# Kernel optimization log

Measured on AMD Instinct MI355X. Metric: run time of the kernel, lower is better.

## Reference

```python
import jax, jax.numpy as jnp
import numpy as np

# ---- fixed problem dims (match init_kwargs) ----
B = 256            # graph pairs
NQ, NC = 96, 120   # nodes per query / corpus graph
EQ, EC = 192, 240  # edges per query / corpus graph
M = 256            # max_edge_set_size (pad target)
RAW = 32           # raw node/edge feature dim
H = 64             # node_state_dim
MSG = 128          # message_dim == encoded edge dim
SDIM = 64          # sinkhorn_feature_dim
PROP_STEPS = 3
TIME_STEPS = 2
SINK_ITERS = 10
TEMP = 0.1
N_NODES = B * (NQ + NC)
N_EDGES = B * (EQ + EC)


def _mlp2(x, W1, b1, W2, b2):
    return jax.nn.relu(x @ W1 + b1) @ W2 + b2


def _split_and_stack(ef):
    # edges laid out [q0, c0, q1, c1, ...]; pad each graph's edges to M
    D = ef.shape[-1]
    ef = ef.reshape(B, EQ + EC, D)
    q = jnp.pad(ef[:, :EQ], ((0, 0), (0, M - EQ), (0, 0)))
    c = jnp.pad(ef[:, EQ:], ((0, 0), (0, M - EC), (0, 0)))
    return q, c


def _sinkhorn(log_alpha):
    la = log_alpha / TEMP
    for _ in range(SINK_ITERS):
        la = la - jax.nn.logsumexp(la, axis=2, keepdims=True)
        la = la - jax.nn.logsumexp(la, axis=1, keepdims=True)
    return jnp.exp(la)


def setup_inputs() -> dict:
    key = jax.random.key(0)
    ks = jax.random.split(key, 16)
    rng = np.random.default_rng(0)
    nodes_per_graph = np.tile(np.array([NQ, NC]), B)            # [2B]
    node_offsets = np.concatenate([[0], np.cumsum(nodes_per_graph)[:-1]])
    edges_per_graph = np.tile(np.array([EQ, EC]), B)
    eg = np.repeat(np.arange(2 * B), edges_per_graph)           # graph id per edge
    from_idx = node_offsets[eg] + rng.integers(0, nodes_per_graph[eg])
    to_idx = node_offsets[eg] + rng.integers(0, nodes_per_graph[eg])

    def lin(k, i, o):
        return (jax.random.normal(k, (i, o), jnp.float32) / np.sqrt(i)).astype(jnp.float32)

    return {
        "node_features": jax.random.normal(ks[0], (N_NODES, RAW), jnp.float32),
        "edge_features": jax.random.normal(ks[1], (N_EDGES, RAW), jnp.float32),
        "from_idx": jnp.asarray(from_idx, jnp.int32),
        "to_idx": jnp.asarray(to_idx, jnp.int32),
        "enc_node_W": lin(ks[2], RAW, H), "enc_node_b": jnp.zeros((H,), jnp.float32),
        "enc_edge_W": lin(ks[3], RAW, MSG), "enc_edge_b": jnp.zeros((MSG,), jnp.float32),
        "msg_W1": lin(ks[4], 2 * H + MSG, 2 * MSG), "msg_b1": jnp.zeros((2 * MSG,), jnp.float32),
        "msg_W2": lin(ks[5], 2 * MSG, MSG), "msg_b2": jnp.zeros((MSG,), jnp.float32),
        "upd_W1": lin(ks[6], H + 2 * MSG, 2 * H), "upd_b1": jnp.zeros((2 * H,), jnp.float32),
        "upd_W2": lin(ks[7], 2 * H, H), "upd_b2": jnp.zeros((H,), jnp.float32),
        "int_W1": lin(ks[8], 2 * MSG, 2 * MSG), "int_b1": jnp.zeros((2 * MSG,), jnp.float32),
        "int_W2": lin(ks[9], 2 * MSG, MSG), "int_b2": jnp.zeros((MSG,), jnp.float32),
        "sink_W1": lin(ks[10], MSG, SDIM), "sink_b1": jnp.zeros((SDIM,), jnp.float32),
        "sink_W2": lin(ks[11], SDIM, SDIM), "sink_b2": jnp.zeros((SDIM,), jnp.float32),
    }


def _forward(node_features, edge_features,
             enc_node_W, enc_node_b, enc_edge_W, enc_edge_b,
             msg_W1, msg_b1, msg_W2, msg_b2,
             upd_W1, upd_b1, upd_W2, upd_b2,
             int_W1, int_b1, int_W2, int_b2,
             sink_W1, sink_b1, sink_W2, sink_b2,
             from_idx, to_idx):
    h0 = node_features @ enc_node_W + enc_node_b      # GraphEncoder (nodes)
    e0 = edge_features @ enc_edge_W + enc_edge_b      # GraphEncoder (edges) -> MSG dim
    mask_q = (jnp.arange(M) < EQ).astype(h0.dtype)[None, :, None]
    mask_c = (jnp.arange(M) < EC).astype(h0.dtype)[None, :, None]

    def edge_msgs(h, comb):
        hf, ht = h[from_idx], h[to_idx]
        mf = _mlp2(jnp.concatenate([hf, ht, comb], -1), msg_W1, msg_b1, msg_W2, msg_b2)
        mb = _mlp2(jnp.concatenate([ht, hf, comb], -1), msg_W1, msg_b1, msg_W2, msg_b2)
        return mf, mb

    plan = None
    q_store = c_store = None
    for _ in range(TIME_STEPS):
        h, e = h0, e0
        inter = jnp.zeros((N_EDGES, MSG), e0.dtype)
        for _ in range(PROP_STEPS):
            # interaction encoder on [edge_features_enc, interaction_features]
            comb = _mlp2(jnp.concatenate([e, inter], -1), int_W1, int_b1, int_W2, int_b2)
            # prop_layer: bidirectional messages + aggregation + node update
            mf, mb = edge_msgs(h, comb)
            agg_f = jax.ops.segment_sum(mf, to_idx, num_segments=N_NODES)
            agg_b = jax.ops.segment_sum(mb, from_idx, num_segments=N_NODES)
            h = _mlp2(jnp.concatenate([h, agg_f, agg_b], -1), upd_W1, upd_b1, upd_W2, upd_b2)
            # propagation_messages: per-edge messages from updated node states
            mf2, mb2 = edge_msgs(h, comb)
            e = mf2 + mb2
            # interaction features via transport-plan gather (zeros on first time step)
            if plan is None:
                inter = jnp.zeros((N_EDGES, MSG), e.dtype)
            else:
                qs, cs = _split_and_stack(e)
                q_int = jnp.einsum('bqc,bcd->bqd', plan, cs)[:, :EQ]
                c_int = jnp.einsum('bqc,bqd->bcd', plan, qs)[:, :EC]
                inter = jnp.concatenate([q_int, c_int], 1).reshape(N_EDGES, MSG)
        q_store, c_store = _split_and_stack(e)
        fq = _mlp2(q_store, sink_W1, sink_b1, sink_W2, sink_b2) * mask_q
        fc = _mlp2(c_store, sink_W1, sink_b1, sink_W2, sink_b2) * mask_c
        plan = _sinkhorn(jnp.einsum('bqd,bcd->bqc', fq, fc))
    # feature_alignment_score: -||Q - P C||_1 per pair
    return -jnp.abs(q_store - jnp.einsum('bqc,bcd->bqd', plan, c_store)).sum((1, 2))


def reference(node_features, edge_features, from_idx, to_idx,
              enc_node_W, enc_node_b, enc_edge_W, enc_edge_b,
              msg_W1, msg_b1, msg_W2, msg_b2,
              upd_W1, upd_b1, upd_W2, upd_b2,
              int_W1, int_b1, int_W2, int_b2,
              sink_W1, sink_b1, sink_W2, sink_b2):
    return _forward(node_features, edge_features,
                    enc_node_W, enc_node_b, enc_edge_W, enc_edge_b,
                    msg_W1, msg_b1, msg_W2, msg_b2,
                    upd_W1, upd_b1, upd_W2, upd_b2,
                    int_W1, int_b1, int_W2, int_b2,
                    sink_W1, sink_b1, sink_W2, sink_b2,
                    from_idx, to_idx)
```

## Files before the change

kernel.cpp:

```cpp
#include <hip/hip_runtime.h>
#include <math.h>

constexpr int BATCH = 256;
constexpr int EQ_   = 192;
constexpr int EC_   = 240;
constexpr int EPG   = 432;
constexpr int NPG   = 216;
constexpr int NN    = BATCH * NPG;
constexpr int NE    = BATCH * EPG;

typedef __attribute__((ext_vector_type(8))) short short8;
typedef __attribute__((ext_vector_type(4))) float floatx4;
typedef unsigned short u16;

__device__ __forceinline__ u16 f2bf(float x) {
  union { float f; unsigned u; } c; c.f = x;
  const unsigned r = (c.u + 0x7FFFu + ((c.u >> 16) & 1u)) >> 16;
  return (u16)r;
}
__device__ __forceinline__ float bf2f(u16 x) {
  union { unsigned u; float f; } c; c.u = ((unsigned)x) << 16;
  return c.f;
}
__device__ __forceinline__ unsigned pack2(float a, float b) {
  return (unsigned)f2bf(a) | ((unsigned)f2bf(b) << 16);
}
__device__ __forceinline__ short8 cvt8(const float* __restrict__ p) {
  const float4 a = *(const float4*)p;
  const float4 b = *(const float4*)(p + 4);
  short8 o;
  o[0]=(short)f2bf(a.x); o[1]=(short)f2bf(a.y); o[2]=(short)f2bf(a.z); o[3]=(short)f2bf(a.w);
  o[4]=(short)f2bf(b.x); o[5]=(short)f2bf(b.y); o[6]=(short)f2bf(b.z); o[7]=(short)f2bf(b.w);
  return o;
}

__device__ __forceinline__ void lse_online(float& m, float& s, float tt) {
  if (tt > m) { s = s * __expf(m - tt) + 1.f; m = tt; }
  else        { s += __expf(tt - m); }
}

__global__ __launch_bounds__(256)
void wconv(const float* __restrict__ W, u16* __restrict__ out, int K, int N)
{
  const int i = blockIdx.x * 256 + threadIdx.x;
  if (i < K * N) {
    const int n = i / K, k = i - n * K;
    out[i] = f2bf(W[(size_t)k * N + n]);
  }
}

template<int K1, int HID, int NOUT, int IN_MODE, int DUAL, int OUT_MODE, int WAVES>
__global__ __launch_bounds__(WAVES * 64, 4)
void mlp_mfma(const void* __restrict__ X, const void* __restrict__ P2,
              const void* __restrict__ P3, const u16* __restrict__ CB,
              const int* __restrict__ IA, const int* __restrict__ IB,
              const u16* __restrict__ W1t, const float* __restrict__ B1,
              const u16* __restrict__ W2t, const float* __restrict__ B2,
              float* __restrict__ Yf, u16* __restrict__ Yb0, u16* __restrict__ Yb1)
{
  constexpr int RT  = 32;
  constexpr int THREADS = WAVES * 64;
  constexpr int KCH = K1 / 8;
  constexpr int NT1 = HID / (WAVES * 16);
  constexpr int NT2 = (NOUT / (WAVES * 16) > 0) ? NOUT / (WAVES * 16) : 1;
  constexpr int SAB = RT * K1 * 2;
  constexpr int SHB = RT * (HID + 8) * 2;
  __shared__ __align__(16) char smem[(SAB > SHB ? SAB : SHB)];
  u16* sA = (u16*)smem;
  u16* sH = (u16*)smem;

  const int tid = threadIdx.x;
  const int rowBase = blockIdx.x * RT;

  for (int ch = tid; ch < RT * KCH; ch += THREADS) {
    const int r = ch / KCH, kc = ch - r * KCH;
    const int gr = rowBase + r, k0 = kc * 8;
    short8 pk;
    if constexpr (IN_MODE == 4) {
      const float* Xf  = (const float*)X;
      const float* P2f = (const float*)P2;
      if (k0 < 128)      pk = cvt8(&Xf[(size_t)gr * 128 + k0]);
      else if (P2f)      pk = cvt8(&P2f[(size_t)gr * 128 + (k0 - 128)]);
      else { pk = short8{0,0,0,0,0,0,0,0}; }
    } else if constexpr (IN_MODE == 1) {
      const u16* Hb = (const u16*)X;
      if (k0 < 64)       pk = *(const short8*)&Hb[(size_t)IA[gr] * 64 + k0];
      else if (k0 < 128) pk = *(const short8*)&Hb[(size_t)IB[gr] * 64 + (k0 - 64)];
      else               pk = *(const short8*)&CB[(size_t)gr * 128 + (k0 - 128)];
    } else {
      const u16* Hb = (const u16*)X;
      const u16* A0 = (const u16*)P2;
      const u16* A1 = (const u16*)P3;
      if (k0 < 64)       pk = *(const short8*)&Hb[(size_t)gr * 64 + k0];
      else if (k0 < 192) pk = *(const short8*)&A0[(size_t)gr * 128 + (k0 - 64)];
      else               pk = *(const short8*)&A1[(size_t)gr * 128 + (k0 - 192)];
    }
    const int byte = ((r * K1 + k0) * 2) ^ ((r & 7) << 4);
    *(short8*)((char*)sA + byte) = pk;
  }
  __syncthreads();

  const int wid = tid >> 6, lane = tid & 63;
  const int l15 = lane & 15, lg = lane >> 4;

  floatx4 acc1[1 + DUAL][2][NT1];
  #pragma unroll
  for (int d = 0; d <= DUAL; ++d)
    #pragma unroll
    for (int m = 0; m < 2; ++m)
      #pragma unroll
      for (int n = 0; n < NT1; ++n) acc1[d][m][n] = floatx4{0.f,0.f,0.f,0.f};

  #pragma unroll 2
  for (int kk = 0; kk < K1 / 32; ++kk) {
    short8 bw[NT1];
    #pragma unroll
    for (int n = 0; n < NT1; ++n) {
      const int col = wid * (HID / WAVES) + n * 16 + l15;
      bw[n] = *(const short8*)&W1t[(size_t)col * K1 + kk * 32 + lg * 8];
    }
    #pragma unroll
    for (int d = 0; d <= DUAL; ++d) {
      int k0 = kk * 32 + lg * 8;
      if (DUAL && d && k0 < 128) k0 ^= 64;
      #pragma unroll
      for (int m = 0; m < 2; ++m) {
        const int r = m * 16 + l15;
        const int byte = ((r * K1 + k0) * 2) ^ ((r & 7) << 4);
        const short8 af = *(const short8*)((char*)sA + byte);
        #pragma unroll
        for (int n = 0; n < NT1; ++n)
          acc1[d][m][n] = __builtin_amdgcn_mfma_f32_16x16x32_bf16(af, bw[n], acc1[d][m][n], 0, 0, 0);
      }
    }
  }
  __syncthreads();

  floatx4 accO[2][NT2];
  #pragma unroll
  for (int m = 0; m < 2; ++m)
    #pragma unroll
    for (int n = 0; n < NT2; ++n) accO[m][n] = floatx4{0.f,0.f,0.f,0.f};

  #pragma unroll
  for (int d = 0; d <= DUAL; ++d) {
    #pragma unroll
    for (int n = 0; n < NT1; ++n) {
      const int col = wid * (HID / WAVES) + n * 16 + l15;
      const float b1 = B1[col];
      #pragma unroll
      for (int m = 0; m < 2; ++m)
        #pragma unroll
        for (int r = 0; r < 4; ++r) {
          const int row = m * 16 + lg * 4 + r;
          const float y = acc1[d][m][n][r] + b1;
          sH[row * (HID + 8) + col] = f2bf(y > 0.f ? y : 0.f);
        }
    }
    __syncthreads();
    if (OUT_MODE == 2 && d == 1) {
      #pragma unroll
      for (int m = 0; m < 2; ++m)
        #pragma unroll
        for (int n = 0; n < NT2; ++n) accO[m][n] = floatx4{0.f,0.f,0.f,0.f};
    }
    #pragma unroll 2
    for (int kk = 0; kk < HID / 32; ++kk) {
      short8 bw2[NT2];
      #pragma unroll
      for (int n = 0; n < NT2; ++n) {
        const int col = wid * (NOUT / WAVES) + n * 16 + l15;
        bw2[n] = *(const short8*)&W2t[(size_t)col * HID + kk * 32 + lg * 8];
      }
      #pragma unroll
      for (int m = 0; m < 2; ++m) {
        const short8 af = *(const short8*)&sH[(m * 16 + l15) * (HID + 8) + kk * 32 + lg * 8];
        #pragma unroll
        for (int n = 0; n < NT2; ++n)
          accO[m][n] = __builtin_amdgcn_mfma_f32_16x16x32_bf16(af, bw2[n], accO[m][n], 0, 0, 0);
      }
    }
    if constexpr (OUT_MODE == 2) {
      u16* Y = d ? Yb1 : Yb0;
      #pragma unroll
      for (int n = 0; n < NT2; ++n) {
        const int col = wid * (NOUT / WAVES) + n * 16 + l15;
        const float b2 = B2[col];
        #pragma unroll
        for (int m = 0; m < 2; ++m)
          #pragma unroll
          for (int r = 0; r < 4; ++r) {
            const int gr = rowBase + m * 16 + lg * 4 + r;
            Y[(size_t)gr * NOUT + col] = f2bf(accO[m][n][r] + b2);
          }
      }
    }
    if (DUAL && d == 0) __syncthreads();
  }

  if constexpr (OUT_MODE != 2) {
    #pragma unroll
    for (int n = 0; n < NT2; ++n) {
      const int col = wid * (NOUT / WAVES) + n * 16 + l15;
      const float b2 = B2[col] * (float)(1 + DUAL);
      #pragma unroll
      for (int m = 0; m < 2; ++m)
        #pragma unroll
        for (int r = 0; r < 4; ++r) {
          const int gr = rowBase + m * 16 + lg * 4 + r;
          const float y = accO[m][n][r] + b2;
          if constexpr (OUT_MODE == 1) {
            Yb0[(size_t)gr * NOUT + col] = f2bf(y);
          } else {
            Yf[(size_t)gr * NOUT + col] = y;
            if constexpr (OUT_MODE == 3)
              Yb0[(size_t)gr * NOUT + col] = f2bf(y);
          }
        }
    }
  }
}

template<int EBF16>
__global__ __launch_bounds__(512, 4)
void comb_msg_fused(const void* __restrict__ E, const u16* __restrict__ INTER,
                    const u16* __restrict__ Hb,
                    const int* __restrict__ IA, const int* __restrict__ IB,
                    const u16* __restrict__ Wi1, const float* __restrict__ Bi1,
                    const u16* __restrict__ Wi2, const float* __restrict__ Bi2,
                    const u16* __restrict__ Wm1, const float* __restrict__ Bm1,
                    const u16* __restrict__ Wm2, const float* __restrict__ Bm2,
                    u16* __restrict__ COMB, u16* __restrict__ MI)
{
  constexpr int RT = 32;
  __shared__ __align__(16) char smem[RT * (256 + 8) * 2];
  u16* sA = (u16*)smem;
  u16* sH = (u16*)smem;

  const int tid = threadIdx.x;
  const int rowBase = blockIdx.x * RT;
  const int wid = tid >> 6, lane = tid & 63;
  const int l15 = lane & 15, lg = lane >> 4;

  for (int ch = tid; ch < RT * 32; ch += 512) {
    const int r = ch >> 5, kc = ch & 31;
    const int gr = rowBase + r, k0 = kc * 8;
    short8 pk;
    if (k0 < 128) {
      if constexpr (EBF16) pk = *(const short8*)&((const u16*)E)[(size_t)gr * 128 + k0];
      else                 pk = cvt8(&((const float*)E)[(size_t)gr * 128 + k0]);
    }
    else if (INTER) pk = *(const short8*)&INTER[(size_t)gr * 128 + (k0 - 128)];
    else            pk = short8{0,0,0,0,0,0,0,0};
    const int byte = ((r * 256 + k0) * 2) ^ ((r & 7) << 4);
    *(short8*)((char*)sA + byte) = pk;
  }
  __syncthreads();

  floatx4 c1[2][2];
  #pragma unroll
  for (int m = 0; m < 2; ++m) { c1[m][0] = floatx4{0,0,0,0}; c1[m][1] = floatx4{0,0,0,0}; }
  #pragma unroll 2
  for (int kk = 0; kk < 8; ++kk) {
    short8 bw[2];
    #pragma unroll
    for (int n = 0; n < 2; ++n) {
      const int col = wid * 32 + n * 16 + l15;
      bw[n] = *(const short8*)&Wi1[(size_t)col * 256 + kk * 32 + lg * 8];
    }
    #pragma unroll
    for (int m = 0; m < 2; ++m) {
      const int r = m * 16 + l15;
      const int byte = ((r * 256 + kk * 32 + lg * 8) * 2) ^ ((r & 7) << 4);
      const short8 af = *(const short8*)((char*)sA + byte);
      c1[m][0] = __builtin_amdgcn_mfma_f32_16x16x32_bf16(af, bw[0], c1[m][0], 0, 0, 0);
      c1[m][1] = __builtin_amdgcn_mfma_f32_16x16x32_bf16(af, bw[1], c1[m][1], 0, 0, 0);
    }
  }
  __syncthreads();
  #pragma unroll
  for (int n = 0; n < 2; ++n) {
    const int col = wid * 32 + n * 16 + l15;
    const float b1 = Bi1[col];
    #pragma unroll
    for (int m = 0; m < 2; ++m)
      #pragma unroll
      for (int r = 0; r < 4; ++r) {
        const int row = m * 16 + lg * 4 + r;
        const float y = c1[m][n][r] + b1;
        sH[row * 264 + col] = f2bf(y > 0.f ? y : 0.f);
      }
  }
  __syncthreads();
  floatx4 cO[2];
  cO[0] = floatx4{0,0,0,0}; cO[1] = floatx4{0,0,0,0};
  #pragma unroll 2
  for (int kk = 0; kk < 8; ++kk) {
    const int col = wid * 16 + l15;
    const short8 bw2 = *(const short8*)&Wi2[(size_t)col * 256 + kk * 32 + lg * 8];
    #pragma unroll
    for (int m = 0; m < 2; ++m) {
      const short8 af = *(const short8*)&sH[(m * 16 + l15) * 264 + kk * 32 + lg * 8];
      cO[m] = __builtin_amdgcn_mfma_f32_16x16x32_bf16(af, bw2, cO[m], 0, 0, 0);
    }
  }
  __syncthreads();

  {
    const int col = wid * 16 + l15;
    const float b2 = Bi2[col];
    #pragma unroll
    for (int m = 0; m < 2; ++m)
      #pragma unroll
      for (int r = 0; r < 4; ++r) {
        const int row = m * 16 + lg * 4 + r;
        const int gr = rowBase + row;
        const u16 v = f2bf(cO[m][r] + b2);
        COMB[(size_t)gr * 128 + col] = v;
        const int k0 = 128 + col;
        const int byte = ((row * 256 + k0) * 2) ^ ((row & 7) << 4);
        *(u16*)((char*)sA + byte) = v;
      }
  }
  for (int ch = tid; ch < RT * 16; ch += 512) {
    const int r = ch >> 4, kc = ch & 15;
    const int gr = rowBase + r, k0 = kc * 8;
    short8 pk;
    if (k0 < 64) pk = *(const short8*)&Hb[(size_t)IA[gr] * 64 + k0];
    else         pk = *(const short8*)&Hb[(size_t)IB[gr] * 64 + (k0 - 64)];
    const int byte = ((r * 256 + k0) * 2) ^ ((r & 7) << 4);
    *(short8*)((char*)sA + byte) = pk;
  }
  __syncthreads();

  floatx4 m1[2][2][2];
  #pragma unroll
  for (int d = 0; d < 2; ++d)
    #pragma unroll
    for (int m = 0; m < 2; ++m) { m1[d][m][0] = floatx4{0,0,0,0}; m1[d][m][1] = floatx4{0,0,0,0}; }
  #pragma unroll 2
  for (int kk = 0; kk < 8; ++kk) {
    short8 bw[2];
    #pragma unroll
    for (int n = 0; n < 2; ++n) {
      const int col = wid * 32 + n * 16 + l15;
      bw[n] = *(const short8*)&Wm1[(size_t)col * 256 + kk * 32 + lg * 8];
    }
    #pragma unroll
    for (int d = 0; d < 2; ++d) {
      int k0 = kk * 32 + lg * 8;
      if (d && k0 < 128) k0 ^= 64;
      #pragma unroll
      for (int m = 0; m < 2; ++m) {
        const int r = m * 16 + l15;
        const int byte = ((r * 256 + k0) * 2) ^ ((r & 7) << 4);
        const short8 af = *(const short8*)((char*)sA + byte);
        m1[d][m][0] = __builtin_amdgcn_mfma_f32_16x16x32_bf16(af, bw[0], m1[d][m][0], 0, 0, 0);
        m1[d][m][1] = __builtin_amdgcn_mfma_f32_16x16x32_bf16(af, bw[1], m1[d][m][1], 0, 0, 0);
      }
    }
  }
  __syncthreads();

  floatx4 mO[2];
  #pragma unroll
  for (int d = 0; d < 2; ++d) {
    #pragma unroll
    for (int n = 0; n < 2; ++n) {
      const int col = wid * 32 + n * 16 + l15;
      const float b1 = Bm1[col];
      #pragma unroll
      for (int m = 0; m < 2; ++m)
        #pragma unroll
        for (int r = 0; r < 4; ++r) {
          const int row = m * 16 + lg * 4 + r;
          const float y = m1[d][m][n][r] + b1;
          sH[row * 264 + col] = f2bf(y > 0.f ? y : 0.f);
        }
    }
    __syncthreads();
    mO[0] = floatx4{0,0,0,0}; mO[1] = floatx4{0,0,0,0};
    #pragma unroll 2
    for (int kk = 0; kk < 8; ++kk) {
      const int col = wid * 16 + l15;
      const short8 bw2 = *(const short8*)&Wm2[(size_t)col * 256 + kk * 32 + lg * 8];
      #pragma unroll
      for (int m = 0; m < 2; ++m) {
        const short8 af = *(const short8*)&sH[(m * 16 + l15) * 264 + kk * 32 + lg * 8];
        mO[m] = __builtin_amdgcn_mfma_f32_16x16x32_bf16(af, bw2, mO[m], 0, 0, 0);
      }
    }
    {
      const int col = wid * 16 + l15;
      const float b2 = Bm2[col];
      #pragma unroll
      for (int m = 0; m < 2; ++m)
        #pragma unroll
        for (int r = 0; r < 4; ++r) {
          const int gr = rowBase + m * 16 + lg * 4 + r;
          MI[(size_t)gr * 256 + d * 128 + col] = f2bf(mO[m][r] + b2);
        }
    }
    if (d == 0) __syncthreads();
  }
}

__global__ __launch_bounds__(512)
void scatter_agg(const u16* __restrict__ MI,
                 const int* __restrict__ FI, const int* __restrict__ TI,
                 u16* __restrict__ AggF, u16* __restrict__ AggB)
{
  const int pair = blockIdx.x >> 1, dir = blockIdx.x & 1;
  const int* SI = dir ? FI : TI;
  u16* Agg      = dir ? AggB : AggF;
  const int tid = threadIdx.x;
  __shared__ float sAgg[NPG * 128];

  for (int i = tid; i < NPG * 128; i += 512) sAgg[i] = 0.f;
  __syncthreads();

  for (int i = tid; i < EPG * 32; i += 512) {
    const int edge = i >> 5, cb = i & 31;
    const int er = pair * EPG + edge;
    const int node = SI[er] - pair * NPG;
    const size_t base = (size_t)er * 256 + dir * 128 + cb;
    #pragma unroll
    for (int k = 0; k < 4; ++k)
      atomicAdd(&sAgg[node * 128 + cb + 32 * k], bf2f(MI[base + 32 * k]));
  }
  __syncthreads();
  unsigned* dst = (unsigned*)(Agg + (size_t)pair * NPG * 128);
  for (int i = tid; i < NPG * 64; i += 512)
    dst[i] = pack2(sAgg[2 * i], sAgg[2 * i + 1]);
}

template<int K1, int HID, int NOUT, int IN_MODE, int SINGLE, int OUTBF>
__global__ __launch_bounds__(256)
void fused_mlp(const float* __restrict__ X, const float* __restrict__ P1,
               const float* __restrict__ W1, const float* __restrict__ B1,
               const float* __restrict__ W2, const float* __restrict__ B2,
               float* __restrict__ Y, u16* __restrict__ Yb, int maskLen)
{
  constexpr int RT = 32, BK = 32;
  constexpr int J1 = HID / 32;
  constexpr int J2 = NOUT / 32;
  constexpr int BMAX = (HID > NOUT ? HID : NOUT);
  __shared__ float sA[RT * 33];
  __shared__ float sB[BK * BMAX];
  __shared__ float sH[SINGLE ? 1 : RT * (HID + 1)];

  const int t  = threadIdx.x;
  const int tx = t & 31, ty = t >> 5;
  const int rowBase = blockIdx.x * RT;

  float acc[4][J1];
  #pragma unroll
  for (int i = 0; i < 4; ++i)
    #pragma unroll
    for (int j = 0; j < J1; ++j) acc[i][j] = 0.f;

  for (int kb = 0; kb < K1; kb += BK) {
    for (int l = t; l < RT * BK; l += 256) {
      const int r = l >> 5, k = l & 31;
      const int gr = rowBase + r, gk = kb + k;
      float v;
      if constexpr (IN_MODE == 0) {
        v = X[(size_t)gr * K1 + gk];
      } else {
        const int bb = gr >> 8, m = gr & 255;
        constexpr int off = (IN_MODE == 5) ? 0 : EQ_;
        constexpr int len = (IN_MODE == 5) ? EQ_ : EC_;
        v = (m < len) ? P1[((size_t)bb * EPG + off + m) * 128 + gk] : 0.f;
      }
      sA[r * 33 + k] = v;
    }
    for (int l = t * 4; l < BK * HID; l += 1024) {
      *(float4*)&sB[l] = *(const float4*)&W1[(size_t)(kb + l / HID) * HID + (l % HID)];
    }
    __syncthreads();
    #pragma unroll
    for (int k = 0; k < BK; ++k) {
      const float a0 = sA[(ty*4+0)*33+k], a1 = sA[(ty*4+1)*33+k],
                  a2 = sA[(ty*4+2)*33+k], a3 = sA[(ty*4+3)*33+k];
      #pragma unroll
      for (int j = 0; j < J1; ++j) {
        const float bb = sB[k * HID + tx + 32*j];
        acc[0][j] += a0 * bb; acc[1][j] += a1 * bb;
        acc[2][j] += a2 * bb; acc[3][j] += a3 * bb;
      }
    }
    __syncthreads();
  }

  if constexpr (SINGLE) {
    #pragma unroll
    for (int j = 0; j < J1; ++j) {
      const int col = tx + 32*j;
      const float bias = B1[col];
      #pragma unroll
      for (int i = 0; i < 4; ++i) {
        const int gr = rowBase + ty*4 + i;
        if constexpr (OUTBF) Yb[(size_t)gr * HID + col] = f2bf(acc[i][j] + bias);
        else                 Y[(size_t)gr * HID + col] = acc[i][j] + bias;
      }
    }
  } else {
    #pragma unroll
    for (int j = 0; j < J1; ++j) {
      const int col = tx + 32*j;
      const float bias = B1[col];
      #pragma unroll
      for (int i = 0; i < 4; ++i) {
        float y = acc[i][j] + bias;
        sH[(ty*4+i) * (HID+1) + col] = y > 0.f ? y : 0.f;
      }
    }
    __syncthreads();

    float acc2[4][J2];
    #pragma unroll
    for (int i = 0; i < 4; ++i)
      #pragma unroll
      for (int j = 0; j < J2; ++j) acc2[i][j] = 0.f;

    for (int kb = 0; kb < HID; kb += BK) {
      for (int l = t * 4; l < BK * NOUT; l += 1024) {
        *(float4*)&sB[l] = *(const float4*)&W2[(size_t)(kb + l / NOUT) * NOUT + (l % NOUT)];
      }
      __syncthreads();
      #pragma unroll
      for (int k = 0; k < BK; ++k) {
        const float a0 = sH[(ty*4+0)*(HID+1) + kb + k],
                    a1 = sH[(ty*4+1)*(HID+1) + kb + k],
                    a2 = sH[(ty*4+2)*(HID+1) + kb + k],
                    a3 = sH[(ty*4+3)*(HID+1) + kb + k];
        #pragma unroll
        for (int j = 0; j < J2; ++j) {
          const float bb = sB[k * NOUT + tx + 32*j];
          acc2[0][j] += a0 * bb; acc2[1][j] += a1 * bb;
          acc2[2][j] += a2 * bb; acc2[3][j] += a3 * bb;
        }
      }
      __syncthreads();
    }
    #pragma unroll
    for (int j = 0; j < J2; ++j) {
      const int col = tx + 32*j;
      const float bias = B2[col];
      #pragma unroll
      for (int i = 0; i < 4; ++i) {
        const int gr = rowBase + ty*4 + i;
        float y = acc2[i][j] + bias;
        if (maskLen >= 0 && (gr & 255) >= maskLen) y = 0.f;
        Y[(size_t)gr * NOUT + col] = y;
      }
    }
  }
}

__global__ __launch_bounds__(256)
void gemm_nt_scale(const float* __restrict__ A, const float* __restrict__ Bm,
                   float* __restrict__ C, float scale)
{
  const int b = blockIdx.z, qt = blockIdx.x, ct = blockIdx.y;
  __shared__ float sA[64 * 68];
  __shared__ float sB[64 * 68];
  const int t = threadIdx.x;
  const int tx = t & 15, ty = t >> 4;
  const float* Ab = A  + (size_t)b * 16384 + (size_t)qt * 4096;
  const float* Bb = Bm + (size_t)b * 16384 + (size_t)ct * 4096;
  for (int l = t * 4; l < 64 * 64; l += 1024) {
    const int r = l >> 6, d = l & 63;
    *(float4*)&sA[r*68 + d] = *(const float4*)&Ab[r*64 + d];
    *(float4*)&sB[r*68 + d] = *(const float4*)&Bb[r*64 + d];
  }
  __syncthreads();
  float acc[4][4] = {};
  #pragma unroll
  for (int d = 0; d < 64; ++d) {
    float a[4], bb[4];
    #pragma unroll
    for (int i = 0; i < 4; ++i) a[i]  = sA[(ty*4+i)*68 + d];
    #pragma unroll
    for (int j = 0; j < 4; ++j) bb[j] = sB[(tx+16*j)*68 + d];
    #pragma unroll
    for (int i = 0; i < 4; ++i)
      #pragma unroll
      for (int j = 0; j < 4; ++j) acc[i][j] += a[i] * bb[j];
  }
  float* Cb = C + (size_t)b * 65536 + (size_t)(qt*64) * 256 + ct*64;
  #pragma unroll
  for (int i = 0; i < 4; ++i)
    #pragma unroll
    for (int j = 0; j < 4; ++j)
      Cb[(ty*4+i)*256 + tx + 16*j] = acc[i][j] * scale;
}

template<int TRANSA, int EBF16, int OUTBF>
__global__ __launch_bounds__(256)
void gemm_plan_mfma(const float* __restrict__ P, const void* __restrict__ E,
                    void* __restrict__ Y, int RPB, int YOFF, int VOFF,
                    int VLEN, int maskRows)
{
  __shared__ u16 sP[64 * 40];
  __shared__ u16 sVT[128 * 40];
  const int b = blockIdx.y, rt = blockIdx.x;
  const int t = threadIdx.x;
  const int wid = t >> 6, lane = t & 63;
  const int l15 = lane & 15, lg = lane >> 4;
  const float* Pb = P + (size_t)b * 65536;

  floatx4 acc[8];
  #pragma unroll
  for (int n = 0; n < 8; ++n) acc[n] = floatx4{0.f,0.f,0.f,0.f};

  for (int kb = 0; kb < 256; kb += 32) {
    if constexpr (TRANSA == 0) {
      for (int l = t; l < 64 * 32; l += 256) {
        const int r = l >> 5, k = l & 31;
        sP[r * 40 + k] = f2bf(Pb[(size_t)(rt * 64 + r) * 256 + kb + k]);
      }
    } else {
      for (int l = t; l < 64 * 32; l += 256) {
        const int q = l >> 6, c = l & 63;
        sP[c * 40 + q] = f2bf(Pb[(size_t)(kb + q) * 256 + rt * 64 + c]);
      }
    }
    for (int l = t; l < 32 * 128; l += 256) {
      const int k = l >> 7, d = l & 127;
      const int vr = kb + k;
      u16 v = 0;
      if (vr < VLEN) {
        if constexpr (EBF16) v = ((const u16*)E)[((size_t)b * EPG + VOFF + vr) * 128 + d];
        else                 v = f2bf(((const float*)E)[((size_t)b * EPG + VOFF + vr) * 128 + d]);
      }
      sVT[d * 40 + k] = v;
    }
    __syncthreads();
    const short8 af = *(const short8*)&sP[(wid * 16 + l15) * 40 + lg * 8];
    #pragma unroll
    for (int n = 0; n < 8; ++n) {
      const short8 bw = *(const short8*)&sVT[(n * 16 + l15) * 40 + lg * 8];
      acc[n] = __builtin_amdgcn_mfma_f32_16x16x32_bf16(af, bw, acc[n], 0, 0, 0);
    }
    __syncthreads();
  }
  #pragma unroll
  for (int n = 0; n < 8; ++n) {
    const int col = n * 16 + l15;
    #pragma unroll
    for (int r = 0; r < 4; ++r) {
      const int row = rt * 64 + wid * 16 + lg * 4 + r;
      if (row < maskRows) {
        const size_t idx = ((size_t)b * RPB + YOFF + row) * 128 + col;
        if constexpr (OUTBF) ((u16*)Y)[idx] = f2bf(acc[n][r]);
        else                 ((float*)Y)[idx] = acc[n][r];
      }
    }
  }
}

__global__ __launch_bounds__(1024)
void sinkhorn_fused(float* __restrict__ S)
{
  const int b = blockIdx.x, t = threadIdx.x;
  float* Sb = S + (size_t)b * 65536;
  const int w = t >> 6, lane = t & 63;
  const int cbase = lane * 4;
  __shared__ float pm[16 * 256], ps[16 * 256];
  __shared__ float su[256], sv[256];
  if (t < 256) sv[t] = 0.f;
  __syncthreads();

  for (int it = 0; it < 10; ++it) {
    const float4 v4 = *(const float4*)&sv[cbase];
    float4 cm = {-1e30f, -1e30f, -1e30f, -1e30f};
    float4 cs = {0.f, 0.f, 0.f, 0.f};
    #pragma unroll 2
    for (int i = 0; i < 16; ++i) {
      const int r = w * 16 + i;
      const float4 s4 = *(const float4*)&Sb[(size_t)r * 256 + cbase];
      const float ax = s4.x + v4.x, ay = s4.y + v4.y;
      const float az = s4.z + v4.z, aw = s4.w + v4.w;
      float m = fmaxf(fmaxf(ax, ay), fmaxf(az, aw));
      #pragma unroll
      for (int off = 32; off; off >>= 1) m = fmaxf(m, __shfl_xor(m, off));
      float s = __expf(ax - m) + __expf(ay - m) + __expf(az - m) + __expf(aw - m);
      #pragma unroll
      for (int off = 32; off; off >>= 1) s += __shfl_xor(s, off);
      const float u = -(m + __logf(s));
      if (lane == 0) su[r] = u;
      lse_online(cm.x, cs.x, s4.x + u);
      lse_online(cm.y, cs.y, s4.y + u);
      lse_online(cm.z, cs.z, s4.z + u);
      lse_online(cm.w, cs.w, s4.w + u);
    }
    *(float4*)&pm[w * 256 + cbase] = cm;
    *(float4*)&ps[w * 256 + cbase] = cs;
    __syncthreads();
    if (t < 256) {
      float m = pm[t];
      #pragma unroll
      for (int k = 1; k < 16; ++k) m = fmaxf(m, pm[k * 256 + t]);
      float s = 0.f;
      #pragma unroll
      for (int k = 0; k < 16; ++k) s += ps[k * 256 + t] * __expf(pm[k * 256 + t] - m);
      sv[t] = -(m + __logf(s));
    }
    __syncthreads();
  }
  for (int i = t; i < 16384; i += 1024) {
    const int row = i >> 6, c4 = (i & 63) * 4;
    float4 s4 = *(float4*)&Sb[(size_t)row * 256 + c4];
    const float uu = su[row];
    const float4 v4 = *(const float4*)&sv[c4];
    s4.x = __expf(s4.x + uu + v4.x);
    s4.y = __expf(s4.y + uu + v4.y);
    s4.z = __expf(s4.z + uu + v4.z);
    s4.w = __expf(s4.w + uu + v4.w);
    *(float4*)&Sb[(size_t)row * 256 + c4] = s4;
  }
}

__global__ __launch_bounds__(256)
void escore_kernel(const float* __restrict__ e, const float* __restrict__ pc,
                   float* __restrict__ out)
{
  const int b = blockIdx.x, t = threadIdx.x;
  float acc = 0.f;
  for (int i4 = t; i4 < 8192; i4 += 256) {
    const int flat = i4 * 4;
    const int m = flat >> 7, d = flat & 127;
    float4 p = *(const float4*)&pc[((size_t)b * 256 + m) * 128 + d];
    float4 q = {0.f, 0.f, 0.f, 0.f};
    if (m < EQ_) q = *(const float4*)&e[((size_t)b * EPG + m) * 128 + d];
    acc += fabsf(q.x - p.x) + fabsf(q.y - p.y) + fabsf(q.z - p.z) + fabsf(q.w - p.w);
  }
  __shared__ float red[256];
  red[t] = acc; __syncthreads();
  for (int s2 = 128; s2 > 0; s2 >>= 1) { if (t < s2) red[t] += red[t + s2]; __syncthreads(); }
  if (t == 0) out[b] = -red[0];
}

extern "C" void kernel_launch(void* const* d_in, const int* in_sizes, int n_in,
                              void* d_out, int out_size, void* d_ws, size_t ws_size,
                              hipStream_t stream)
{
  const float* node_features = (const float*)d_in[0];
  const float* edge_features = (const float*)d_in[1];
  const int*   from_idx      = (const int*)d_in[2];
  const int*   to_idx        = (const int*)d_in[3];
  const float* enc_node_W = (const float*)d_in[4];
  const float* enc_node_b = (const float*)d_in[5];
  const float* enc_edge_W = (const float*)d_in[6];
  const float* enc_edge_b = (const float*)d_in[7];
  const float* msg_W1 = (const float*)d_in[8];
  const float* msg_b1 = (const float*)d_in[9];
  const float* msg_W2 = (const float*)d_in[10];
  const float* msg_b2 = (const float*)d_in[11];
  const float* upd_W1 = (const float*)d_in[12];
  const float* upd_b1 = (const float*)d_in[13];
  const float* upd_W2 = (const float*)d_in[14];
  const float* upd_b2 = (const float*)d_in[15];
  const float* int_W1 = (const float*)d_in[16];
  const float* int_b1 = (const float*)d_in[17];
  const float* int_W2 = (const float*)d_in[18];
  const float* int_b2 = (const float*)d_in[19];
  const float* sink_W1 = (const float*)d_in[20];
  const float* sink_b1 = (const float*)d_in[21];
  const float* sink_W2 = (const float*)d_in[22];
  const float* sink_b2 = (const float*)d_in[23];
  float* out = (float*)d_out;

  u16* wsu = (u16*)d_ws;
  u16*   hb  = wsu;
  float* e   = (float*)(wsu + (size_t)NN * 64);
  float* shr = e + (size_t)NE * 128;
  float* S   = shr + (size_t)BATCH * 32768;
  u16* comb  = (u16*)(S + (size_t)BATCH * 65536);
  u16* e1b   = comb + (size_t)NE * 128;
  u16* h1b   = e1b + (size_t)NE * 128;
  u16* wi1 = h1b + (size_t)NN * 64;
  u16* wi2 = wi1 + 65536;
  u16* wm1 = wi2 + 32768;
  u16* wm2 = wm1 + 65536;
  u16* wu1 = wm2 + 32768;
  u16* wu2 = wu1 + 40960;

  u16* mI = (u16*)e;
  u16* interb = (u16*)shr;
  u16* aggFb  = (u16*)shr;
  u16* aggBb  = aggFb + (size_t)NN * 128;
  float* fq   = shr;
  float* fc   = shr + (size_t)BATCH * 16384;
  float* pc   = shr;

  wconv<<<256, 256, 0, stream>>>(int_W1, wi1, 256, 256);
  wconv<<<128, 256, 0, stream>>>(int_W2, wi2, 256, 128);
  wconv<<<256, 256, 0, stream>>>(msg_W1, wm1, 256, 256);
  wconv<<<128, 256, 0, stream>>>(msg_W2, wm2, 256, 128);
  wconv<<<160, 256, 0, stream>>>(upd_W1, wu1, 320, 128);
  wconv<<< 32, 256, 0, stream>>>(upd_W2, wu2, 128, 64);

  fused_mlp<32,64,64,0,1,1><<<NN/32, 256, 0, stream>>>(
      node_features, nullptr, enc_node_W, enc_node_b, nullptr, nullptr,
      nullptr, hb, -1);
  fused_mlp<32,128,128,0,1,0><<<NE/32, 256, 0, stream>>>(
      edge_features, nullptr, enc_edge_W, enc_edge_b, nullptr, nullptr,
      e, nullptr, -1);

  for (int p = 0; p < 3; ++p) {
    comb_msg_fused<0><<<NE/32, 512, 0, stream>>>(
        e, nullptr, hb, from_idx, to_idx,
        wi1, int_b1, wi2, int_b2, wm1, msg_b1, wm2, msg_b2, comb, mI);
    scatter_agg<<<BATCH*2, 512, 0, stream>>>(mI, from_idx, to_idx, aggFb, aggBb);
    mlp_mfma<320,128,64,3,0,1,4><<<NN/32, 256, 0, stream>>>(
        hb, aggFb, aggBb, nullptr, nullptr, nullptr,
        wu1, upd_b1, wu2, upd_b2, nullptr, hb, nullptr);
    if (p == 0) {
      hipMemcpyAsync(h1b, hb, (size_t)NN * 64 * 2, hipMemcpyDeviceToDevice, stream);
      mlp_mfma<256,256,128,1,1,3,8><<<NE/32, 512, 0, stream>>>(
          hb, nullptr, nullptr, comb, from_idx, to_idx,
          wm1, msg_b1, wm2, msg_b2, e, e1b, nullptr);
    } else {
      mlp_mfma<256,256,128,1,1,0,8><<<NE/32, 512, 0, stream>>>(
          hb, nullptr, nullptr, comb, from_idx, to_idx,
          wm1, msg_b1, wm2, msg_b2, e, nullptr, nullptr);
    }
  }
  fused_mlp<128,64,64,5,0,0><<<BATCH*8, 256, 0, stream>>>(
      nullptr, e, sink_W1, sink_b1, sink_W2, sink_b2, fq, nullptr, EQ_);
  fused_mlp<128,64,64,6,0,0><<<BATCH*8, 256, 0, stream>>>(
      nullptr, e, sink_W1, sink_b1, sink_W2, sink_b2, fc, nullptr, EC_);
  gemm_nt_scale<<<dim3(4,4,BATCH), 256, 0, stream>>>(fq, fc, S, 10.0f);
  sinkhorn_fused<<<BATCH, 1024, 0, stream>>>(S);

  hipMemcpyAsync(hb, h1b, (size_t)NN * 64 * 2, hipMemcpyDeviceToDevice, stream);
  gemm_plan_mfma<0,1,1><<<dim3(4, BATCH), 256, 0, stream>>>(
      S, e1b, interb, EPG, 0,   EQ_, EC_, EQ_);
  gemm_plan_mfma<1,1,1><<<dim3(4, BATCH), 256, 0, stream>>>(
      S, e1b, interb, EPG, EQ_, 0,   EQ_, EC_);

  comb_msg_fused<1><<<NE/32, 512, 0, stream>>>(
      e1b, interb, hb, from_idx, to_idx,
      wi1, int_b1, wi2, int_b2, wm1, msg_b1, wm2, msg_b2, comb, mI);
  scatter_agg<<<BATCH*2, 512, 0, stream>>>(mI, from_idx, to_idx, aggFb, aggBb);
  mlp_mfma<320,128,64,3,0,1,4><<<NN/32, 256, 0, stream>>>(
      hb, aggFb, aggBb, nullptr, nullptr, nullptr,
      wu1, upd_b1, wu2, upd_b2, nullptr, hb, nullptr);
  mlp_mfma<256,256,128,1,1,0,8><<<NE/32, 512, 0, stream>>>(
      hb, nullptr, nullptr, comb, from_idx, to_idx,
      wm1, msg_b1, wm2, msg_b2, e, nullptr, nullptr);
  gemm_plan_mfma<0,0,1><<<dim3(4, BATCH), 256, 0, stream>>>(
      S, e, interb, EPG, 0,   EQ_, EC_, EQ_);
  gemm_plan_mfma<1,0,1><<<dim3(4, BATCH), 256, 0, stream>>>(
      S, e, interb, EPG, EQ_, 0,   EQ_, EC_);

  comb_msg_fused<0><<<NE/32, 512, 0, stream>>>(
      e, interb, hb, from_idx, to_idx,
      wi1, int_b1, wi2, int_b2, wm1, msg_b1, wm2, msg_b2, comb, mI);
  scatter_agg<<<BATCH*2, 512, 0, stream>>>(mI, from_idx, to_idx, aggFb, aggBb);
  mlp_mfma<320,128,64,3,0,1,4><<<NN/32, 256, 0, stream>>>(
      hb, aggFb, aggBb, nullptr, nullptr, nullptr,
      wu1, upd_b1, wu2, upd_b2, nullptr, hb, nullptr);
  mlp_mfma<256,256,128,1,1,0,8><<<NE/32, 512, 0, stream>>>(
      hb, nullptr, nullptr, comb, from_idx, to_idx,
      wm1, msg_b1, wm2, msg_b2, e, nullptr, nullptr);

  fused_mlp<128,64,64,5,0,0><<<BATCH*8, 256, 0, stream>>>(
      nullptr, e, sink_W1, sink_b1, sink_W2, sink_b2, fq, nullptr, EQ_);
  fused_mlp<128,64,64,6,0,0><<<BATCH*8, 256, 0, stream>>>(
      nullptr, e, sink_W1, sink_b1, sink_W2, sink_b2, fc, nullptr, EC_);
  gemm_nt_scale<<<dim3(4,4,BATCH), 256, 0, stream>>>(fq, fc, S, 10.0f);
  sinkhorn_fused<<<BATCH, 1024, 0, stream>>>(S);

  gemm_plan_mfma<0,0,0><<<dim3(4, BATCH), 256, 0, stream>>>(
      S, e, pc, 256, 0, EQ_, EC_, 256);
  escore_kernel<<<BATCH, 256, 0, stream>>>(e, pc, out);
}
```

Baseline: 3.492 ms.

## Run Sinkhorn feature MLP on MFMA with split-bf16 and simplify column LSE

Replaces the fp32 SIMT two-layer Sinkhorn feature MLP with an MFMA kernel. It splits both activations and weights into bf16 hi/lo parts and uses three MFMAs per tile to approximate fp32 accuracy. It also drops the online max tracking in the Sinkhorn column logsumexp and sums exp(s+u) directly. This relies on values being bounded after row normalization, which removes per-element branching and max reductions. The risks are a small loss of precision in the MLP and possible underflow or overflow in the column sums.

Measured after the change: 3.271 ms. 6.3% less time.

```diff
diff --git a/kernel.cpp b/kernel.cpp
--- a/kernel.cpp
+++ b/kernel.cpp
@@ -46,6 +46,20 @@
   if (i < K * N) {
     const int n = i / K, k = i - n * K;
     out[i] = f2bf(W[(size_t)k * N + n]);
+  }
+}
+
+__global__ __launch_bounds__(256)
+void wconv_split(const float* __restrict__ W, u16* __restrict__ hi,
+                 u16* __restrict__ lo, int K, int N)
+{
+  const int i = blockIdx.x * 256 + threadIdx.x;
+  if (i < K * N) {
+    const int n = i / K, k = i - n * K;
+    const float w = W[(size_t)k * N + n];
+    const u16 h = f2bf(w);
+    hi[i] = h;
+    lo[i] = f2bf(w - bf2f(h));
   }
 }
 
@@ -504,57 +518,108 @@
         else                 Y[(size_t)gr * HID + col] = acc[i][j] + bias;
       }
     }
-  } else {
-    #pragma unroll
-    for (int j = 0; j < J1; ++j) {
-      const int col = tx + 32*j;
-      const float bias = B1[col];
-      #pragma unroll
-      for (int i = 0; i < 4; ++i) {
-        float y = acc[i][j] + bias;
-        sH[(ty*4+i) * (HID+1) + col] = y > 0.f ? y : 0.f;
-      }
-    }
-    __syncthreads();
-
-    float acc2[4][J2];
-    #pragma unroll
-    for (int i = 0; i < 4; ++i)
-      #pragma unroll
-      for (int j = 0; j < J2; ++j) acc2[i][j] = 0.f;
-
-    for (int kb = 0; kb < HID; kb += BK) {
-      for (int l = t * 4; l < BK * NOUT; l += 1024) {
-        *(float4*)&sB[l] = *(const float4*)&W2[(size_t)(kb + l / NOUT) * NOUT + (l % NOUT)];
-      }
-      __syncthreads();
-      #pragma unroll
-      for (int k = 0; k < BK; ++k) {
-        const float a0 = sH[(ty*4+0)*(HID+1) + kb + k],
-                    a1 = sH[(ty*4+1)*(HID+1) + kb + k],
-                    a2 = sH[(ty*4+2)*(HID+1) + kb + k],
-                    a3 = sH[(ty*4+3)*(HID+1) + kb + k];
-        #pragma unroll
-        for (int j = 0; j < J2; ++j) {
-          const float bb = sB[k * NOUT + tx + 32*j];
-          acc2[0][j] += a0 * bb; acc2[1][j] += a1 * bb;
-          acc2[2][j] += a2 * bb; acc2[3][j] += a3 * bb;
-        }
-      }
-      __syncthreads();
-    }
-    #pragma unroll
-    for (int j = 0; j < J2; ++j) {
-      const int col = tx + 32*j;
-      const float bias = B2[col];
-      #pragma unroll
-      for (int i = 0; i < 4; ++i) {
-        const int gr = rowBase + ty*4 + i;
-        float y = acc2[i][j] + bias;
-        if (maskLen >= 0 && (gr & 255) >= maskLen) y = 0.f;
-        Y[(size_t)gr * NOUT + col] = y;
-      }
-    }
+  }
+}
+
+template<int OFFSET, int LEN>
+__global__ __launch_bounds__(256)
+void sink_mlp_split(const float* __restrict__ E,
+                    const u16* __restrict__ W1hi, const u16* __restrict__ W1lo,
+                    const float* __restrict__ B1,
+                    const u16* __restrict__ W2hi, const u16* __restrict__ W2lo,
+                    const float* __restrict__ B2,
+                    float* __restrict__ Y)
+{
+  __shared__ u16 sAhi[32 * 136], sAlo[32 * 136];
+  __shared__ u16 sHhi[32 * 72],  sHlo[32 * 72];
+  const int tid = threadIdx.x;
+  const int rowBase = blockIdx.x * 32;
+
+  for (int ch = tid; ch < 32 * 16; ch += 256) {
+    const int r = ch >> 4, kc = ch & 15;
+    const int gr = rowBase + r, k0 = kc * 8;
+    const int b = gr >> 8, m = gr & 255;
+    short8 hi, lo;
+    if (m < LEN) {
+      const float* src = &E[((size_t)b * EPG + OFFSET + m) * 128 + k0];
+      #pragma unroll
+      for (int j = 0; j < 8; ++j) {
+        const float v = src[j];
+        const u16 h = f2bf(v);
+        hi[j] = (short)h;
+        lo[j] = (short)f2bf(v - bf2f(h));
+      }
+    } else {
+      hi = short8{0,0,0,0,0,0,0,0};
+      lo = short8{0,0,0,0,0,0,0,0};
+    }
+    *(short8*)&sAhi[r * 136 + k0] = hi;
+    *(short8*)&sAlo[r * 136 + k0] = lo;
+  }
+  __syncthreads();
+
+  const int wid = tid >> 6, lane = tid & 63;
+  const int l15 = lane & 15, lg = lane >> 4;
+  const int col = wid * 16 + l15;
+
+  floatx4 acc[2];
+  acc[0] = floatx4{0,0,0,0}; acc[1] = floatx4{0,0,0,0};
+  #pragma unroll
+  for (int kk = 0; kk < 4; ++kk) {
+    const short8 bh = *(const short8*)&W1hi[(size_t)col * 128 + kk * 32 + lg * 8];
+    const short8 bl = *(const short8*)&W1lo[(size_t)col * 128 + kk * 32 + lg * 8];
+    #pragma unroll
+    for (int m = 0; m < 2; ++m) {
+      const int r = m * 16 + l15;
+      const short8 ahi = *(const short8*)&sAhi[r * 136 + kk * 32 + lg * 8];
+      const short8 alo = *(const short8*)&sAlo[r * 136 + kk * 32 + lg * 8];
+      acc[m] = __builtin_amdgcn_mfma_f32_16x16x32_bf16(ahi, bh, acc[m], 0, 0, 0);
+      acc[m] = __builtin_amdgcn_mfma_f32_16x16x32_bf16(ahi, bl, acc[m], 0, 0, 0);
+      acc[m] = __builtin_amdgcn_mfma_f32_16x16x32_bf16(alo, bh, acc[m], 0, 0, 0);
+    }
+  }
+  {
+    const float b1 = B1[col];
+    #pragma unroll
+    for (int m = 0; m < 2; ++m)
+      #pragma unroll
+      for (int r4 = 0; r4 < 4; ++r4) {
+        const int row = m * 16 + lg * 4 + r4;
+        float y = acc[m][r4] + b1;
+        y = y > 0.f ? y : 0.f;
+        const u16 h = f2bf(y);
+        sHhi[row * 72 + col] = h;
+        sHlo[row * 72 + col] = f2bf(y - bf2f(h));
+      }
+  }
+  __syncthreads();
+  floatx4 acc2[2];
+  acc2[0] = floatx4{0,0,0,0}; acc2[1] = floatx4{0,0,0,0};
+  #pragma unroll
+  for (int kk = 0; kk < 2; ++kk) {
+    const short8 bh = *(const short8*)&W2hi[(size_t)col * 64 + kk * 32 + lg * 8];
+    const short8 bl = *(const short8*)&W2lo[(size_t)col * 64 + kk * 32 + lg * 8];
+    #pragma unroll
+    for (int m = 0; m < 2; ++m) {
+      const int r = m * 16 + l15;
+      const short8 ahi = *(const short8*)&sHhi[r * 72 + kk * 32 + lg * 8];
+      const short8 alo = *(const short8*)&sHlo[r * 72 + kk * 32 + lg * 8];
+      acc2[m] = __builtin_amdgcn_mfma_f32_16x16x32_bf16(ahi, bh, acc2[m], 0, 0, 0);
+      acc2[m] = __builtin_amdgcn_mfma_f32_16x16x32_bf16(ahi, bl, acc2[m], 0, 0, 0);
+      acc2[m] = __builtin_amdgcn_mfma_f32_16x16x32_bf16(alo, bh, acc2[m], 0, 0, 0);
+    }
+  }
+  {
+    const float b2 = B2[col];
+    #pragma unroll
+    for (int m = 0; m < 2; ++m)
+      #pragma unroll
+      for (int r4 = 0; r4 < 4; ++r4) {
+        const int gr = rowBase + m * 16 + lg * 4 + r4;
+        float y = acc2[m][r4] + b2;
+        if ((gr & 255) >= LEN) y = 0.f;
+        Y[(size_t)gr * 64 + col] = y;
+      }
   }
 }
 
@@ -667,14 +732,13 @@
   float* Sb = S + (size_t)b * 65536;
   const int w = t >> 6, lane = t & 63;
   const int cbase = lane * 4;
-  __shared__ float pm[16 * 256], ps[16 * 256];
+  __shared__ float ps[16 * 256];
   __shared__ float su[256], sv[256];
   if (t < 256) sv[t] = 0.f;
   __syncthreads();
 
   for (int it = 0; it < 10; ++it) {
     const float4 v4 = *(const float4*)&sv[cbase];
-    float4 cm = {-1e30f, -1e30f, -1e30f, -1e30f};
     float4 cs = {0.f, 0.f, 0.f, 0.f};
     #pragma unroll 2
     for (int i = 0; i < 16; ++i) {
@@ -690,22 +754,18 @@
       for (int off = 32; off; off >>= 1) s += __shfl_xor(s, off);
       const float u = -(m + __logf(s));
       if (lane == 0) su[r] = u;
-      lse_online(cm.x, cs.x, s4.x + u);
-      lse_online(cm.y, cs.y, s4.y + u);
-      lse_online(cm.z, cs.z, s4.z + u);
-      lse_online(cm.w, cs.w, s4.w + u);
-    }
-    *(float4*)&pm[w * 256 + cbase] = cm;
+      cs.x += __expf(s4.x + u);
+      cs.y += __expf(s4.y + u);
+      cs.z += __expf(s4.z + u);
+      cs.w += __expf(s4.w + u);
+    }
     *(float4*)&ps[w * 256 + cbase] = cs;
     __syncthreads();
     if (t < 256) {
-      float m = pm[t];
-      #pragma unroll
-      for (int k = 1; k < 16; ++k) m = fmaxf(m, pm[k * 256 + t]);
       float s = 0.f;
       #pragma unroll
-      for (int k = 0; k < 16; ++k) s += ps[k * 256 + t] * __expf(pm[k * 256 + t] - m);
-      sv[t] = -(m + __logf(s));
+      for (int k = 0; k < 16; ++k) s += ps[k * 256 + t];
+      sv[t] = -__logf(fmaxf(s, 1e-38f));
     }
     __syncthreads();
   }
@@ -786,6 +846,10 @@
   u16* wm2 = wm1 + 65536;
   u16* wu1 = wm2 + 32768;
   u16* wu2 = wu1 + 40960;
+  u16* ws1h = wu2 + 8192;
+  u16* ws1l = ws1h + 8192;
+  u16* ws2h = ws1l + 8192;
+  u16* ws2l = ws2h + 4096;
 
   u16* mI = (u16*)e;
   u16* interb = (u16*)shr;
@@ -801,6 +865,8 @@
   wconv<<<128, 256, 0, stream>>>(msg_W2, wm2, 256, 128);
   wconv<<<160, 256, 0, stream>>>(upd_W1, wu1, 320, 128);
   wconv<<< 32, 256, 0, stream>>>(upd_W2, wu2, 128, 64);
+  wconv_split<<<32, 256, 0, stream>>>(sink_W1, ws1h, ws1l, 128, 64);
+  wconv_split<<<16, 256, 0, stream>>>(sink_W2, ws2h, ws2l, 64, 64);
 
   fused_mlp<32,64,64,0,1,1><<<NN/32, 256, 0, stream>>>(
       node_features, nullptr, enc_node_W, enc_node_b, nullptr, nullptr,
@@ -828,10 +894,10 @@
           wm1, msg_b1, wm2, msg_b2, e, nullptr, nullptr);
     }
   }
-  fused_mlp<128,64,64,5,0,0><<<BATCH*8, 256, 0, stream>>>(
-      nullptr, e, sink_W1, sink_b1, sink_W2, sink_b2, fq, nullptr, EQ_);
-  fused_mlp<128,64,64,6,0,0><<<BATCH*8, 256, 0, stream>>>(
-      nullptr, e, sink_W1, sink_b1, sink_W2, sink_b2, fc, nullptr, EC_);
+  sink_mlp_split<0,   EQ_><<<BATCH*8, 256, 0, stream>>>(
+      e, ws1h, ws1l, sink_b1, ws2h, ws2l, sink_b2, fq);
+  sink_mlp_split<EQ_, EC_><<<BATCH*8, 256, 0, stream>>>(
+      e, ws1h, ws1l, sink_b1, ws2h, ws2l, sink_b2, fc);
   gemm_nt_scale<<<dim3(4,4,BATCH), 256, 0, stream>>>(fq, fc, S, 10.0f);
   sinkhorn_fused<<<BATCH, 1024, 0, stream>>>(S);
 
@@ -867,10 +933,10 @@
       hb, nullptr, nullptr, comb, from_idx, to_idx,
       wm1, msg_b1, wm2, msg_b2, e, nullptr, nullptr);
 
-  fused_mlp<128,64,64,5,0,0><<<BATCH*8, 256, 0, stream>>>(
-      nullptr, e, sink_W1, sink_b1, sink_W2, sink_b2, fq, nullptr, EQ_);
-  fused_mlp<128,64,64,6,0,0><<<BATCH*8, 256, 0, stream>>>(
-      nullptr, e, sink_W1, sink_b1, sink_W2, sink_b2, fc, nullptr, EC_);
+  sink_mlp_split<0,   EQ_><<<BATCH*8, 256, 0, stream>>>(
+      e, ws1h, ws1l, sink_b1, ws2h, ws2l, sink_b2, fq);
+  sink_mlp_split<EQ_, EC_><<<BATCH*8, 256, 0, stream>>>(
+      e, ws1h, ws1l, sink_b1, ws2h, ws2l, sink_b2, fc);
   gemm_nt_scale<<<dim3(4,4,BATCH), 256, 0, stream>>>(fq, fc, S, 10.0f);
   sinkhorn_fused<<<BATCH, 1024, 0, stream>>>(S);
 
```
